# Optimization experiments

Hardware: AMD Instinct MI355X
Metric: run time of the kernel (lower is better)

The kernel has to match this reference:

```python
import jax, jax.numpy as jnp
import numpy as np

WEIGHT = 0.1


def setup_inputs() -> dict:
    key = jax.random.key(0)
    phases = jax.random.normal(key, (8, 8192, 256), dtype=jnp.float32)  # [B, S, C]
    return {"phases": phases}


def reference(phases) -> jnp.ndarray:
    # Original: diff = phases[:, :, None] - phases[:, None, :]; loss = weight * mean(diff**2)
    # Identity: mean_{i,j} (x_i - x_j)^2 over the seq axis equals 2 * Var_i(x)
    # (biased variance), so the O(S^2) pairwise tensor never needs to exist.
    # loss = weight * 2 * mean over (b, c) of Var over seq axis.
    var_seq = jnp.var(phases, axis=1)          # [B, C], biased (divide by S)
    return jnp.asarray(WEIGHT, phases.dtype) * 2.0 * jnp.mean(var_seq)
```

## Files before the change

kernel.cpp:

```cpp
#include <hip/hip_runtime.h>

#define BB 8
#define SS 8192
#define CC 256

#define NBLK 256
#define CPB (NBLK / BB)
#define SCHUNK (SS / CPB)
#define NW 16
#define ITERS (SCHUNK / NW)


__global__ __launch_bounds__(1024) void pcl_partial(const float* __restrict__ x,
                                                    float* __restrict__ ws1,
                                                    float* __restrict__ ws2) {
    const int blk   = blockIdx.x;
    const int b     = blk >> 5;
    const int chunk = blk & 31;
    const int s0    = chunk * SCHUNK;
    const int t = threadIdx.x;
    const int w = t >> 6;
    const int l = t & 63;

    const float4* p = reinterpret_cast<const float4*>(
        x + ((size_t)b * SS + (size_t)(s0 + w)) * CC) + l;

    float sx0 = 0.f, sx1 = 0.f, sx2 = 0.f, sx3 = 0.f, sq = 0.f;
    #pragma unroll 8
    for (int k = 0; k < ITERS; ++k) {
        float4 v = p[(size_t)k * (NW * CC / 4)];
        sx0 += v.x; sx1 += v.y; sx2 += v.z; sx3 += v.w;
        sq  += v.x * v.x + v.y * v.y + v.z * v.z + v.w * v.w;
    }

    __shared__ float lsum[NW][CC];
    *reinterpret_cast<float4*>(&lsum[w][l * 4]) = make_float4(sx0, sx1, sx2, sx3);

    for (int off = 32; off > 0; off >>= 1) sq += __shfl_down(sq, off, 64);
    __shared__ float x2buf[NW];
    if (l == 0) x2buf[w] = sq;
    __syncthreads();

    if (t < CC) {
        float col = 0.f;
        #pragma unroll
        for (int g = 0; g < NW; ++g) col += lsum[g][t];
        ws1[blk * CC + t] = col;
    }
    if (t == 0) {
        float s2 = 0.f;
        #pragma unroll
        for (int g = 0; g < NW; ++g) s2 += x2buf[g];
        ws2[blk] = s2;
    }
}

__global__ __launch_bounds__(1024) void pcl_final(const float* __restrict__ ws1,
                                                  const float* __restrict__ ws2,
                                                  float* __restrict__ out) {
    const int t = threadIdx.x;
    float P = 0.f;

    if (t < 512) {
        const int b  = t >> 6;
        const int cq = t & 63;
        const float4* p4 = reinterpret_cast<const float4*>(ws1)
                           + (size_t)(b * CPB) * (CC / 4) + cq;
        float4 s = make_float4(0.f, 0.f, 0.f, 0.f);
        #pragma unroll 8
        for (int ch = 0; ch < CPB; ++ch) {
            float4 v = p4[(size_t)ch * (CC / 4)];
            s.x += v.x; s.y += v.y; s.z += v.z; s.w += v.w;
        }
        const float inv_s = 1.0f / SS;
        const float m0 = s.x * inv_s, m1 = s.y * inv_s,
                    m2 = s.z * inv_s, m3 = s.w * inv_s;
        P = -(m0 * m0 + m1 * m1 + m2 * m2 + m3 * m3) * (1.0f / (BB * CC));
    } else if (t < 512 + NBLK) {
        P = ws2[t - 512] * (1.0f / ((float)BB * SS * CC));
    }

    for (int off = 32; off > 0; off >>= 1) P += __shfl_down(P, off, 64);
    __shared__ float buf[16];
    if ((t & 63) == 0) buf[t >> 6] = P;
    __syncthreads();
    if (t == 0) {
        float tot = 0.f;
        #pragma unroll
        for (int i = 0; i < 16; ++i) tot += buf[i];
        out[0] = 0.2f * tot;
    }
}

extern "C" void kernel_launch(void* const* d_in, const int* in_sizes, int n_in,
                              void* d_out, int out_size, void* d_ws, size_t ws_size,
                              hipStream_t stream) {
    const float* x = (const float*)d_in[0];
    float* ws1 = (float*)d_ws;
    float* ws2 = ws1 + NBLK * CC;
    float* out = (float*)d_out;

    pcl_partial<<<NBLK, 1024, 0, stream>>>(x, ws1, ws2);
    pcl_final<<<1, 1024, 0, stream>>>(ws1, ws2, out);
}
```

Measured before the change: 21.00 us.

## Split final reduction into 32-block mid stage plus tiny final kernel

Replaces the single-block final reduction over the 256x256 partial sums with a 32-block middle kernel that reduces each (batch, 64-channel) slice. A 64-thread final kernel then sums the 32 results. The main loop is also fully unrolled. The aim is to spread the serial final reduction across more CUs, at the cost of an extra kernel launch.

Result: slower. 21.73 us (+3.5%).

```diff
diff --git a/kernel.cpp b/kernel.cpp
--- a/kernel.cpp
+++ b/kernel.cpp
@@ -26,7 +26,7 @@
         x + ((size_t)b * SS + (size_t)(s0 + w)) * CC) + l;
 
     float sx0 = 0.f, sx1 = 0.f, sx2 = 0.f, sx3 = 0.f, sq = 0.f;
-    #pragma unroll 8
+    #pragma unroll
     for (int k = 0; k < ITERS; ++k) {
         float4 v = p[(size_t)k * (NW * CC / 4)];
         sx0 += v.x; sx1 += v.y; sx2 += v.z; sx3 += v.w;
@@ -55,41 +55,41 @@
     }
 }
 
-__global__ __launch_bounds__(1024) void pcl_final(const float* __restrict__ ws1,
-                                                  const float* __restrict__ ws2,
-                                                  float* __restrict__ out) {
-    const int t = threadIdx.x;
-    float P = 0.f;
+__global__ __launch_bounds__(256) void pcl_mid(const float* __restrict__ ws1,
+                                               const float* __restrict__ ws2,
+                                               float* __restrict__ ws3) {
+    const int k  = blockIdx.x;
+    const int b  = k >> 2;
+    const int c0 = (k & 3) * 64;
+    const int t  = threadIdx.x;
+    const int w  = t >> 6;
+    const int l  = t & 63;
 
-    if (t < 512) {
-        const int b  = t >> 6;
-        const int cq = t & 63;
-        const float4* p4 = reinterpret_cast<const float4*>(ws1)
-                           + (size_t)(b * CPB) * (CC / 4) + cq;
-        float4 s = make_float4(0.f, 0.f, 0.f, 0.f);
-        #pragma unroll 8
-        for (int ch = 0; ch < CPB; ++ch) {
-            float4 v = p4[(size_t)ch * (CC / 4)];
-            s.x += v.x; s.y += v.y; s.z += v.z; s.w += v.w;
-        }
-        const float inv_s = 1.0f / SS;
-        const float m0 = s.x * inv_s, m1 = s.y * inv_s,
-                    m2 = s.z * inv_s, m3 = s.w * inv_s;
-        P = -(m0 * m0 + m1 * m1 + m2 * m2 + m3 * m3) * (1.0f / (BB * CC));
-    } else if (t < 512 + NBLK) {
-        P = ws2[t - 512] * (1.0f / ((float)BB * SS * CC));
+    const float* base = ws1 + (size_t)(b * CPB + w * 8) * CC + c0 + l;
+    float s = 0.f;
+    #pragma unroll
+    for (int j = 0; j < 8; ++j) s += base[(size_t)j * CC];
+
+    __shared__ float sL[4][64];
+    sL[w][l] = s;
+    __syncthreads();
+
+    if (t < 64) {
+        const float col = sL[0][t] + sL[1][t] + sL[2][t] + sL[3][t];
+        const float m   = col * (1.0f / SS);
+        float P = -m * m * (1.0f / (BB * CC));
+        if (t < 8) P += ws2[k * 8 + t] * (1.0f / ((float)BB * SS * CC));
+        for (int off = 32; off > 0; off >>= 1) P += __shfl_down(P, off, 64);
+        if (t == 0) ws3[k] = P;
     }
+}
 
+__global__ __launch_bounds__(64) void pcl_final(const float* __restrict__ ws3,
+                                                float* __restrict__ out) {
+    const int l = threadIdx.x;
+    float P = (l < 32) ? ws3[l] : 0.f;
     for (int off = 32; off > 0; off >>= 1) P += __shfl_down(P, off, 64);
-    __shared__ float buf[16];
-    if ((t & 63) == 0) buf[t >> 6] = P;
-    __syncthreads();
-    if (t == 0) {
-        float tot = 0.f;
-        #pragma unroll
-        for (int i = 0; i < 16; ++i) tot += buf[i];
-        out[0] = 0.2f * tot;
-    }
+    if (l == 0) out[0] = 0.2f * P;
 }
 
 extern "C" void kernel_launch(void* const* d_in, const int* in_sizes, int n_in,
@@ -98,8 +98,10 @@
     const float* x = (const float*)d_in[0];
     float* ws1 = (float*)d_ws;
     float* ws2 = ws1 + NBLK * CC;
+    float* ws3 = ws2 + NBLK;
     float* out = (float*)d_out;
 
     pcl_partial<<<NBLK, 1024, 0, stream>>>(x, ws1, ws2);
-    pcl_final<<<1, 1024, 0, stream>>>(ws1, ws2, out);
+    pcl_mid<<<32, 256, 0, stream>>>(ws1, ws2, ws3);
+    pcl_final<<<1, 64, 0, stream>>>(ws3, out);
 }
```

## Fuse partial and final reductions into one cooperative kernel with grid sync

Applied to the files above, without the earlier changes.

Merges the two kernels into one cooperative launch. Block 0 performs the final reduction after a grid-wide barrier, which removes the second kernel launch and its gap. The main loop is also fully unrolled and the sum of squares is split into two accumulators to shorten the dependency chain. Cooperative launch adds the cost of a grid barrier and requires all 256 blocks of 1024 threads to be co-resident.

After: 57.67 us. 2.75x slower.

```diff
diff --git a/kernel.cpp b/kernel.cpp
--- a/kernel.cpp
+++ b/kernel.cpp
@@ -1,4 +1,7 @@
 #include <hip/hip_runtime.h>
+#include <hip/hip_cooperative_groups.h>
+
+namespace cg = cooperative_groups;
 
 #define BB 8
 #define SS 8192
@@ -11,9 +14,10 @@
 #define ITERS (SCHUNK / NW)
 
 
-__global__ __launch_bounds__(1024) void pcl_partial(const float* __restrict__ x,
-                                                    float* __restrict__ ws1,
-                                                    float* __restrict__ ws2) {
+__global__ __launch_bounds__(1024) void pcl_fused(const float* __restrict__ x,
+                                                  float* __restrict__ ws1,
+                                                  float* __restrict__ ws2,
+                                                  float* __restrict__ out) {
     const int blk   = blockIdx.x;
     const int b     = blk >> 5;
     const int chunk = blk & 31;
@@ -25,13 +29,16 @@
     const float4* p = reinterpret_cast<const float4*>(
         x + ((size_t)b * SS + (size_t)(s0 + w)) * CC) + l;
 
-    float sx0 = 0.f, sx1 = 0.f, sx2 = 0.f, sx3 = 0.f, sq = 0.f;
-    #pragma unroll 8
+    float sx0 = 0.f, sx1 = 0.f, sx2 = 0.f, sx3 = 0.f;
+    float sqa = 0.f, sqb = 0.f;
+    #pragma unroll
     for (int k = 0; k < ITERS; ++k) {
         float4 v = p[(size_t)k * (NW * CC / 4)];
         sx0 += v.x; sx1 += v.y; sx2 += v.z; sx3 += v.w;
-        sq  += v.x * v.x + v.y * v.y + v.z * v.z + v.w * v.w;
+        sqa += v.x * v.x + v.y * v.y;
+        sqb += v.z * v.z + v.w * v.w;
     }
+    float sq = sqa + sqb;
 
     __shared__ float lsum[NW][CC];
     *reinterpret_cast<float4*>(&lsum[w][l * 4]) = make_float4(sx0, sx1, sx2, sx3);
@@ -53,19 +60,17 @@
         for (int g = 0; g < NW; ++g) s2 += x2buf[g];
         ws2[blk] = s2;
     }
-}
 
-__global__ __launch_bounds__(1024) void pcl_final(const float* __restrict__ ws1,
-                                                  const float* __restrict__ ws2,
-                                                  float* __restrict__ out) {
-    const int t = threadIdx.x;
+    cg::this_grid().sync();
+
+    if (blk != 0) return;
+
     float P = 0.f;
-
     if (t < 512) {
-        const int b  = t >> 6;
+        const int bb = t >> 6;
         const int cq = t & 63;
         const float4* p4 = reinterpret_cast<const float4*>(ws1)
-                           + (size_t)(b * CPB) * (CC / 4) + cq;
+                           + (size_t)(bb * CPB) * (CC / 4) + cq;
         float4 s = make_float4(0.f, 0.f, 0.f, 0.f);
         #pragma unroll 8
         for (int ch = 0; ch < CPB; ++ch) {
@@ -81,13 +86,14 @@
     }
 
     for (int off = 32; off > 0; off >>= 1) P += __shfl_down(P, off, 64);
-    __shared__ float buf[16];
+    __shared__ float buf[NW];
+    __syncthreads();
     if ((t & 63) == 0) buf[t >> 6] = P;
     __syncthreads();
     if (t == 0) {
         float tot = 0.f;
         #pragma unroll
-        for (int i = 0; i < 16; ++i) tot += buf[i];
+        for (int i = 0; i < NW; ++i) tot += buf[i];
         out[0] = 0.2f * tot;
     }
 }
@@ -100,6 +106,7 @@
     float* ws2 = ws1 + NBLK * CC;
     float* out = (float*)d_out;
 
-    pcl_partial<<<NBLK, 1024, 0, stream>>>(x, ws1, ws2);
-    pcl_final<<<1, 1024, 0, stream>>>(ws1, ws2, out);
+    void* args[] = {(void*)&x, (void*)&ws1, (void*)&ws2, (void*)&out};
+    hipLaunchCooperativeKernel((const void*)pcl_fused, dim3(NBLK), dim3(1024),
+                               args, 0, stream);
 }
```

## Repartition blocks by channel slice and sequence half to shrink partial workspace

Applied to the files above, without the earlier changes.

Each block now covers a 16-channel slice over half of the sequence instead of all 256 channels over a 256-row chunk. Column sums are reduced with wavefront shuffles instead of a shared-memory table, so only 2×2048 partial sums go to the workspace. The final kernel then does one float4 load pair per thread with 512 threads instead of looping over 32 chunks. The trade-off is a less coalesced read: each row is touched in 64-byte pieces strided by 1 KB, which may waste DRAM or cache-line bandwidth on the main pass.

Result: slower. 28.35 us (+35.0%).

```diff
diff --git a/kernel.cpp b/kernel.cpp
--- a/kernel.cpp
+++ b/kernel.cpp
@@ -5,47 +5,64 @@
 #define CC 256
 
 #define NBLK 256
-#define CPB (NBLK / BB)
-#define SCHUNK (SS / CPB)
+#define HALF (SS / 2)
 #define NW 16
-#define ITERS (SCHUNK / NW)
+#define PASSES (HALF / 256)
 
 
 __global__ __launch_bounds__(1024) void pcl_partial(const float* __restrict__ x,
                                                     float* __restrict__ ws1,
                                                     float* __restrict__ ws2) {
-    const int blk   = blockIdx.x;
-    const int b     = blk >> 5;
-    const int chunk = blk & 31;
-    const int s0    = chunk * SCHUNK;
+    const int blk = blockIdx.x;
+    const int b   = blk >> 5;
+    const int r   = blk & 31;
+    const int cs  = r >> 1;
+    const int sh  = r & 1;
     const int t = threadIdx.x;
     const int w = t >> 6;
     const int l = t & 63;
+    const int rq = t >> 2;
+    const int cq = t & 3;
 
-    const float4* p = reinterpret_cast<const float4*>(
-        x + ((size_t)b * SS + (size_t)(s0 + w)) * CC) + l;
+    const float4* p = reinterpret_cast<const float4*>(x)
+        + ((size_t)b * SS + (size_t)sh * HALF + rq) * (CC / 4) + cs * 4 + cq;
 
-    float sx0 = 0.f, sx1 = 0.f, sx2 = 0.f, sx3 = 0.f, sq = 0.f;
-    #pragma unroll 8
-    for (int k = 0; k < ITERS; ++k) {
-        float4 v = p[(size_t)k * (NW * CC / 4)];
-        sx0 += v.x; sx1 += v.y; sx2 += v.z; sx3 += v.w;
-        sq  += v.x * v.x + v.y * v.y + v.z * v.z + v.w * v.w;
+    float4 s4 = make_float4(0.f, 0.f, 0.f, 0.f);
+    float sqa = 0.f, sqb = 0.f;
+    #pragma unroll
+    for (int k = 0; k < PASSES; ++k) {
+        float4 v = p[(size_t)k * 256 * (CC / 4)];
+        s4.x += v.x; s4.y += v.y; s4.z += v.z; s4.w += v.w;
+        sqa += v.x * v.x + v.y * v.y;
+        sqb += v.z * v.z + v.w * v.w;
     }
 
-    __shared__ float lsum[NW][CC];
-    *reinterpret_cast<float4*>(&lsum[w][l * 4]) = make_float4(sx0, sx1, sx2, sx3);
+    for (int off = 32; off >= 4; off >>= 1) {
+        s4.x += __shfl_down(s4.x, off, 64);
+        s4.y += __shfl_down(s4.y, off, 64);
+        s4.z += __shfl_down(s4.z, off, 64);
+        s4.w += __shfl_down(s4.w, off, 64);
+    }
+    __shared__ float4 wsum[NW][4];
+    if (l < 4) wsum[w][l] = s4;
 
+    float sq = sqa + sqb;
     for (int off = 32; off > 0; off >>= 1) sq += __shfl_down(sq, off, 64);
     __shared__ float x2buf[NW];
     if (l == 0) x2buf[w] = sq;
     __syncthreads();
 
-    if (t < CC) {
-        float col = 0.f;
-        #pragma unroll
-        for (int g = 0; g < NW; ++g) col += lsum[g][t];
-        ws1[blk * CC + t] = col;
+    if (t < 64) {
+        const int wv = t >> 2, c = t & 3;
+        float4 v = wsum[wv][c];
+        for (int off = 32; off >= 4; off >>= 1) {
+            v.x += __shfl_down(v.x, off, 64);
+            v.y += __shfl_down(v.y, off, 64);
+            v.z += __shfl_down(v.z, off, 64);
+            v.w += __shfl_down(v.w, off, 64);
+        }
+        if (t < 4)
+            reinterpret_cast<float4*>(ws1)[sh * 512 + b * 64 + cs * 4 + t] = v;
     }
     if (t == 0) {
         float s2 = 0.f;
@@ -55,39 +72,27 @@
     }
 }
 
-__global__ __launch_bounds__(1024) void pcl_final(const float* __restrict__ ws1,
-                                                  const float* __restrict__ ws2,
-                                                  float* __restrict__ out) {
+__global__ __launch_bounds__(512) void pcl_final(const float* __restrict__ ws1,
+                                                 const float* __restrict__ ws2,
+                                                 float* __restrict__ out) {
     const int t = threadIdx.x;
-    float P = 0.f;
-
-    if (t < 512) {
-        const int b  = t >> 6;
-        const int cq = t & 63;
-        const float4* p4 = reinterpret_cast<const float4*>(ws1)
-                           + (size_t)(b * CPB) * (CC / 4) + cq;
-        float4 s = make_float4(0.f, 0.f, 0.f, 0.f);
-        #pragma unroll 8
-        for (int ch = 0; ch < CPB; ++ch) {
-            float4 v = p4[(size_t)ch * (CC / 4)];
-            s.x += v.x; s.y += v.y; s.z += v.z; s.w += v.w;
-        }
-        const float inv_s = 1.0f / SS;
-        const float m0 = s.x * inv_s, m1 = s.y * inv_s,
-                    m2 = s.z * inv_s, m3 = s.w * inv_s;
-        P = -(m0 * m0 + m1 * m1 + m2 * m2 + m3 * m3) * (1.0f / (BB * CC));
-    } else if (t < 512 + NBLK) {
-        P = ws2[t - 512] * (1.0f / ((float)BB * SS * CC));
-    }
+    const float4* w4 = reinterpret_cast<const float4*>(ws1);
+    const float4 a = w4[t];
+    const float4 c = w4[512 + t];
+    const float inv_s = 1.0f / SS;
+    const float m0 = (a.x + c.x) * inv_s, m1 = (a.y + c.y) * inv_s,
+                m2 = (a.z + c.z) * inv_s, m3 = (a.w + c.w) * inv_s;
+    float P = -(m0 * m0 + m1 * m1 + m2 * m2 + m3 * m3) * (1.0f / (BB * CC));
+    if (t < NBLK) P += ws2[t] * (1.0f / ((float)BB * SS * CC));
 
     for (int off = 32; off > 0; off >>= 1) P += __shfl_down(P, off, 64);
-    __shared__ float buf[16];
+    __shared__ float buf[8];
     if ((t & 63) == 0) buf[t >> 6] = P;
     __syncthreads();
     if (t == 0) {
         float tot = 0.f;
         #pragma unroll
-        for (int i = 0; i < 16; ++i) tot += buf[i];
+        for (int i = 0; i < 8; ++i) tot += buf[i];
         out[0] = 0.2f * tot;
     }
 }
@@ -97,9 +102,9 @@
                               hipStream_t stream) {
     const float* x = (const float*)d_in[0];
     float* ws1 = (float*)d_ws;
-    float* ws2 = ws1 + NBLK * CC;
+    float* ws2 = ws1 + 2 * 2048;
     float* out = (float*)d_out;
 
     pcl_partial<<<NBLK, 1024, 0, stream>>>(x, ws1, ws2);
-    pcl_final<<<1, 1024, 0, stream>>>(ws1, ws2, out);
+    pcl_final<<<1, 512, 0, stream>>>(ws1, ws2, out);
 }
```
